# Optimization experiments

Hardware: AMD Instinct MI355X
Metric: run time of the kernel (lower is better)

The kernel has to match this reference:

```python
import jax, jax.numpy as jnp
import numpy as np

D_MODEL = 1024
NUM_HEADS = 16
D_K = D_MODEL // NUM_HEADS


def setup_inputs() -> dict:
    key = jax.random.key(0)
    kq, kk, kv, k1, k2, k3, k4 = jax.random.split(key, 7)
    B, S = 2, 2048
    # Xavier-uniform init for square [d_model, d_model] weights
    limit = float(np.sqrt(6.0 / (D_MODEL + D_MODEL)))
    def xav(k):
        return jax.random.uniform(k, (D_MODEL, D_MODEL), jnp.float32, -limit, limit)
    return {
        "query": jax.random.normal(kq, (B, S, D_MODEL), jnp.float32),
        "key": jax.random.normal(kk, (B, S, D_MODEL), jnp.float32),
        "value": jax.random.normal(kv, (B, S, D_MODEL), jnp.float32),
        "W_q": xav(k1),
        "W_k": xav(k2),
        "W_v": xav(k3),
        "W_o": xav(k4),
    }


def reference(query, key, value, W_q, W_k, W_v, W_o):
    B, Sq, _ = query.shape
    Sk = key.shape[1]
    # Linear layers: y = x @ W.T (torch nn.Linear convention)
    Q = (query @ W_q.T).reshape(B, Sq, NUM_HEADS, D_K).transpose(0, 2, 1, 3)
    K = (key @ W_k.T).reshape(B, Sk, NUM_HEADS, D_K).transpose(0, 2, 1, 3)
    V = (value @ W_v.T).reshape(B, Sk, NUM_HEADS, D_K).transpose(0, 2, 1, 3)
    scale = 1.0 / jnp.sqrt(jnp.asarray(D_K, Q.dtype))
    scores = jnp.einsum("bhqd,bhkd->bhqk", Q, K) * scale  # [B,H,Sq,Sk]
    attn = jax.nn.softmax(scores, axis=-1)
    # dropout is identity in eval mode
    out = jnp.einsum("bhqk,bhkd->bhqd", attn, V)
    out = out.transpose(0, 2, 1, 3).reshape(B, Sq, D_MODEL)
    return out @ W_o.T
```

## Files before the change

kernel.cpp:

```cpp
#include <hip/hip_runtime.h>
#include <math.h>

typedef unsigned short ushort_t;
typedef __attribute__((ext_vector_type(8))) short short8;
typedef __attribute__((ext_vector_type(4))) float f32x4;
typedef __attribute__((ext_vector_type(16))) float f32x16;
typedef __attribute__((ext_vector_type(4))) unsigned short ushort4v;
typedef __attribute__((ext_vector_type(2))) unsigned int uint2v;
typedef __attribute__((ext_vector_type(4))) unsigned int uint4v;

#define D_MODEL 1024
#define SEQ 2048
#define MROWS 4096
#define PLANE (MROWS * D_MODEL)
#define WELEM (D_MODEL * D_MODEL)

static __device__ __forceinline__ ushort_t f2bf(float f) {
    unsigned u = __builtin_bit_cast(unsigned, f);
    return (ushort_t)((u + 0x7fffu + ((u >> 16) & 1u)) >> 16);
}
static __device__ __forceinline__ unsigned cvtpk(float lo, float hi) {
    unsigned r;
    asm("v_cvt_pk_bf16_f32 %0, %1, %2" : "=v"(r) : "v"(lo), "v"(hi));
    return r;
}
static __device__ __forceinline__ short8 cvt8(float4 a, float4 b) {
    uint4v u = {cvtpk(a.x, a.y), cvtpk(a.z, a.w),
                cvtpk(b.x, b.y), cvtpk(b.z, b.w)};
    return __builtin_bit_cast(short8, u);
}

#define GLDS16(gp, lp)                                                         \
    __builtin_amdgcn_global_load_lds(                                          \
        (const __attribute__((address_space(1))) void*)(gp),                   \
        (__attribute__((address_space(3))) void*)(lp), 16, 0, 0)

__global__ __launch_bounds__(256)
void cvt_w(const float* __restrict__ w0, const float* __restrict__ w1,
           const float* __restrict__ w2, const float* __restrict__ w3,
           ushort_t* __restrict__ dst) {
    const int p = blockIdx.x >> 9;
    const float* s = (p == 0) ? w0 : (p == 1) ? w1 : (p == 2) ? w2 : w3;
    const int i = (((int)blockIdx.x & 511) * 256 + threadIdx.x) * 8;
    float4 a = *(const float4*)(s + i);
    float4 bb = *(const float4*)(s + i + 4);
    *(short8*)(dst + (size_t)p * WELEM + i) = cvt8(a, bb);
}

__global__ __launch_bounds__(256, 6)
void gemm3(const float* __restrict__ Xq, const float* __restrict__ Xk,
           const float* __restrict__ Xv, const ushort_t* __restrict__ Wb,
           ushort_t* __restrict__ Cb) {
    __shared__ __align__(16) ushort_t As[64 * 64];
    __shared__ __align__(16) ushort_t Bs[128 * 64];

    const int lin = blockIdx.x + blockIdx.y * 8 + blockIdx.z * 512;
    const int lin2 = (lin & 7) * 192 + (lin >> 3);
    const int z = lin2 >> 9;
    const int rem = lin2 & 511;
    const int by = rem >> 3;
    const int bx = rem & 7;

    const float* A = (z == 0) ? Xq : (z == 1) ? Xk : Xv;
    const ushort_t* B = Wb + (size_t)z * WELEM;
    ushort_t* C = Cb + (size_t)z * PLANE;

    const int tid = threadIdx.x;
    const int lane = tid & 63;
    const int wid = tid >> 6;
    const int wr = wid >> 1, wc = wid & 1;
    const int brow = by * 64;
    const int bcol = bx * 128;

    const int lrow = lane >> 3;
    const int g8 = lane & 7;
    const int loff = (g8 ^ lrow) * 8;

    const float* aF[2];
#pragma unroll
    for (int i = 0; i < 2; ++i)
        aF[i] = A + (size_t)(brow + wid * 16 + i * 8 + lrow) * D_MODEL + loff;
    const ushort_t* bS[4];
#pragma unroll
    for (int i = 0; i < 4; ++i)
        bS[i] = B + (size_t)(bcol + wid * 32 + i * 8 + lrow) * D_MODEL + loff;

    f32x4 acc[2][4];
#pragma unroll
    for (int i = 0; i < 2; ++i)
#pragma unroll
        for (int j = 0; j < 4; ++j) acc[i][j] = {0.f, 0.f, 0.f, 0.f};

    const int fr = lane & 15, fg = lane >> 4;

    float4 ar[2][2];
#pragma unroll
    for (int i = 0; i < 2; ++i) {
        ar[i][0] = *(const float4*)(aF[i]);
        ar[i][1] = *(const float4*)(aF[i] + 4);
    }

    for (int k0 = 0; k0 < D_MODEL; k0 += 64) {
        __syncthreads();
#pragma unroll
        for (int i = 0; i < 2; ++i)
            *(short8*)&As[(wid * 16 + i * 8 + lrow) * 64 + g8 * 8] =
                cvt8(ar[i][0], ar[i][1]);
#pragma unroll
        for (int i = 0; i < 4; ++i)
            GLDS16(bS[i] + k0, Bs + (wid * 32 + i * 8) * 64);
        if (k0 + 64 < D_MODEL) {
#pragma unroll
            for (int i = 0; i < 2; ++i) {
                ar[i][0] = *(const float4*)(aF[i] + k0 + 64);
                ar[i][1] = *(const float4*)(aF[i] + k0 + 68);
            }
        }
        __syncthreads();
#pragma unroll
        for (int ks = 0; ks < 2; ++ks) {
            const int coff = (ks * 32 + fg * 8) ^ ((fr & 7) << 3);
            short8 af[2], bw[4];
#pragma unroll
            for (int mi = 0; mi < 2; ++mi)
                af[mi] = *(const short8*)&As[(wr * 32 + mi * 16 + fr) * 64 + coff];
#pragma unroll
            for (int nj = 0; nj < 4; ++nj)
                bw[nj] = *(const short8*)&Bs[(wc * 64 + nj * 16 + fr) * 64 + coff];
#pragma unroll
            for (int mi = 0; mi < 2; ++mi)
#pragma unroll
                for (int nj = 0; nj < 4; ++nj)
                    acc[mi][nj] = __builtin_amdgcn_mfma_f32_16x16x32_bf16(
                        af[mi], bw[nj], acc[mi][nj], 0, 0, 0);
        }
    }

    if (z < 2) {
#pragma unroll
        for (int mi = 0; mi < 2; ++mi)
#pragma unroll
            for (int nj = 0; nj < 4; ++nj) {
                const int n = bcol + wc * 64 + nj * 16 + fr;
#pragma unroll
                for (int r = 0; r < 4; ++r) {
                    const int m = brow + wr * 32 + mi * 16 + fg * 4 + r;
                    C[(size_t)m * D_MODEL + n] = f2bf(acc[mi][nj][r]);
                }
            }
    } else {
#pragma unroll
        for (int mi = 0; mi < 2; ++mi)
#pragma unroll
            for (int nj = 0; nj < 4; ++nj) {
                const int n = bcol + wc * 64 + nj * 16 + fr;
                const int m0 = brow + wr * 32 + mi * 16 + fg * 4;
                ushort4v o4;
#pragma unroll
                for (int r = 0; r < 4; ++r) o4[r] = f2bf(acc[mi][nj][r]);
                *(ushort4v*)&C[((size_t)(m0 >> 11) << 21) + (size_t)n * SEQ + (m0 & 2047)] = o4;
            }
    }
}

__global__ __launch_bounds__(256)
void gemm_out(const ushort_t* __restrict__ A, const ushort_t* __restrict__ B,
              float* __restrict__ C) {
    __shared__ __align__(16) ushort_t As[2][128 * 64];
    __shared__ __align__(16) ushort_t Bs[2][64 * 64];

    const int lin = blockIdx.x + blockIdx.y * 16;
    const int lin2 = (lin & 7) * 64 + (lin >> 3);
    const int by = lin2 >> 4;
    const int bx = lin2 & 15;

    const int tid = threadIdx.x;
    const int lane = tid & 63;
    const int wid = tid >> 6;
    const int wr = wid >> 1, wc = wid & 1;
    const int brow = by * 128;
    const int bcol = bx * 64;

    const int lrow = lane >> 3;
    const int loff = ((lane & 7) ^ lrow) * 8;

    const ushort_t* aSrc[4];
    const ushort_t* bSrc[2];
#pragma unroll
    for (int i = 0; i < 4; ++i)
        aSrc[i] = A + (size_t)(brow + (wid * 4 + i) * 8 + lrow) * D_MODEL + loff;
#pragma unroll
    for (int i = 0; i < 2; ++i)
        bSrc[i] = B + (size_t)(bcol + (wid * 2 + i) * 8 + lrow) * D_MODEL + loff;

    f32x4 acc[4][2];
#pragma unroll
    for (int i = 0; i < 4; ++i)
#pragma unroll
        for (int j = 0; j < 2; ++j) acc[i][j] = {0.f, 0.f, 0.f, 0.f};

    const int fr = lane & 15, fg = lane >> 4;

#pragma unroll
    for (int i = 0; i < 4; ++i) GLDS16(aSrc[i], As[0] + (wid * 4 + i) * 512);
#pragma unroll
    for (int i = 0; i < 2; ++i) GLDS16(bSrc[i], Bs[0] + (wid * 2 + i) * 512);

    int cur = 0;
    for (int k0 = 0; k0 < D_MODEL; k0 += 64) {
        __syncthreads();
        if (k0 + 64 < D_MODEL) {
#pragma unroll
            for (int i = 0; i < 4; ++i)
                GLDS16(aSrc[i] + k0 + 64, As[cur ^ 1] + (wid * 4 + i) * 512);
#pragma unroll
            for (int i = 0; i < 2; ++i)
                GLDS16(bSrc[i] + k0 + 64, Bs[cur ^ 1] + (wid * 2 + i) * 512);
        }
#pragma unroll
        for (int ks = 0; ks < 2; ++ks) {
            const int coff = (ks * 32 + fg * 8) ^ ((fr & 7) << 3);
            short8 af[4], bw[2];
#pragma unroll
            for (int mi = 0; mi < 4; ++mi)
                af[mi] = *(const short8*)&As[cur][(wr * 64 + mi * 16 + fr) * 64 + coff];
#pragma unroll
            for (int nj = 0; nj < 2; ++nj)
                bw[nj] = *(const short8*)&Bs[cur][(wc * 32 + nj * 16 + fr) * 64 + coff];
#pragma unroll
            for (int mi = 0; mi < 4; ++mi)
#pragma unroll
                for (int nj = 0; nj < 2; ++nj)
                    acc[mi][nj] = __builtin_amdgcn_mfma_f32_16x16x32_bf16(
                        af[mi], bw[nj], acc[mi][nj], 0, 0, 0);
        }
        cur ^= 1;
    }

#pragma unroll
    for (int mi = 0; mi < 4; ++mi)
#pragma unroll
        for (int nj = 0; nj < 2; ++nj) {
            const int n = bcol + wc * 32 + nj * 16 + fr;
#pragma unroll
            for (int r = 0; r < 4; ++r) {
                const int m = brow + wr * 64 + mi * 16 + fg * 4 + r;
                C[(size_t)m * D_MODEL + n] = acc[mi][nj][r];
            }
        }
}

__global__ __launch_bounds__(512, 4)
void attn_mfma(const ushort_t* __restrict__ Qp, const ushort_t* __restrict__ Kp,
               const ushort_t* __restrict__ VT, ushort_t* __restrict__ Ap) {
    __shared__ __align__(16) ushort_t KB[4][4096];
    __shared__ __align__(16) ushort_t VB[4][4096];
    __shared__ float sm[2][128];
    __shared__ float sl[2][128];

    const int tid = threadIdx.x;
    const int lane = tid & 63;
    const int wid = tid >> 6;
    const int qgrp = wid & 3;
    const int khalf = wid >> 2;

    const int bid0 = blockIdx.x;
    const int bid = (bid0 & 7) * 64 + (bid0 >> 3);
    const int qt = bid & 15;
    const int h = (bid >> 4) & 15;
    const int b = bid >> 8;

    const int lrow = lane >> 3;
    const int loff = ((lane & 7) ^ lrow) * 8;
    const int q31 = lane & 31;
    const int hi = lane >> 5;

    const int m0 = b * SEQ + qt * 128;

    ushort_t* Qstage = &KB[2][0];
#pragma unroll
    for (int j = 0; j < 2; ++j) {
        const ushort_t* qS =
            Qp + (size_t)(m0 + wid * 16 + j * 8 + lrow) * D_MODEL + h * 64 + loff;
        GLDS16(qS, Qstage + (wid * 16 + j * 8) * 64);
    }
    const ushort_t* kS =
        Kp + (size_t)(b * SEQ + wid * 8 + lrow) * D_MODEL + h * 64 + loff;
    const ushort_t* vS =
        VT + ((size_t)b << 21) + (size_t)(h * 64 + wid * 8 + lrow) * SEQ + loff;
    GLDS16(kS, KB[0] + wid * 512);
    GLDS16(vS, VB[0] + wid * 512);
    kS += 64 * D_MODEL;
    vS += 64;
    GLDS16(kS, KB[1] + wid * 512);
    GLDS16(vS, VB[1] + wid * 512);
    kS += 64 * D_MODEL;
    vS += 64;
    __syncthreads();

    const int qrow = qgrp * 32 + q31;
    const int rsw = q31 & 7;
    short8 aq[4];
#pragma unroll
    for (int s = 0; s < 4; ++s)
        aq[s] = *(const short8*)&Qstage[qrow * 64 + (((s * 2 + hi) ^ rsw) * 8)];
    __syncthreads();

    f32x16 accO[2];
#pragma unroll
    for (int db = 0; db < 2; ++db)
#pragma unroll
        for (int r = 0; r < 16; ++r) accO[db][r] = 0.f;
    float m_s = -INFINITY;
    float l_p = 0.f;

    const float CEXP = 0.18033688011112042f;
    const int kbase = khalf * 32;

    int cur = 0;
    for (int st = 0; st < SEQ / 128; ++st) {
        if (st + 1 < SEQ / 128) {
            const int b0 = (cur ^ 1) * 2;
            GLDS16(kS, KB[b0] + wid * 512);
            GLDS16(vS, VB[b0] + wid * 512);
            kS += 64 * D_MODEL;
            vS += 64;
            GLDS16(kS, KB[b0 + 1] + wid * 512);
            GLDS16(vS, VB[b0 + 1] + wid * 512);
            kS += 64 * D_MODEL;
            vS += 64;
        }

#pragma unroll
        for (int sub = 0; sub < 2; ++sub) {
            const int bufi = cur * 2 + sub;

            f32x16 accS;
#pragma unroll
            for (int r = 0; r < 16; ++r) accS[r] = 0.f;
            __builtin_amdgcn_s_setprio(1);
#pragma unroll
            for (int s = 0; s < 4; ++s) {
                short8 ak = *(const short8*)&KB[bufi][(kbase + q31) * 64 +
                                                     (((s * 2 + hi) ^ rsw) * 8)];
                accS = __builtin_amdgcn_mfma_f32_32x32x16_bf16(ak, aq[s], accS, 0, 0, 0);
            }
            __builtin_amdgcn_s_setprio(0);

            float mx = accS[0];
#pragma unroll
            for (int r = 1; r < 16; ++r) mx = fmaxf(mx, accS[r]);
            mx = fmaxf(mx, __shfl_xor(mx, 32));
            const float cand = mx * CEXP;
            if (__any(cand > m_s + 8.f)) {
                const float mnew = fmaxf(m_s, cand);
                const float al = __builtin_amdgcn_exp2f(m_s - mnew);
                m_s = mnew;
                l_p *= al;
#pragma unroll
                for (int db = 0; db < 2; ++db)
#pragma unroll
                    for (int r = 0; r < 16; ++r) accO[db][r] *= al;
            }
            float ps = 0.f;
            const float nm = -m_s;
#pragma unroll
            for (int r = 0; r < 16; ++r) {
                const float p = __builtin_amdgcn_exp2f(fmaf(accS[r], CEXP, nm));
                accS[r] = p;
                ps += p;
            }
            l_p += ps;

            short8 pf[2];
#pragma unroll
            for (int ks2 = 0; ks2 < 2; ++ks2) {
                const int bse = ks2 * 8;
                unsigned w0 = cvtpk(accS[bse + 0], accS[bse + 1]);
                unsigned w1 = cvtpk(accS[bse + 2], accS[bse + 3]);
                unsigned w2 = cvtpk(accS[bse + 4], accS[bse + 5]);
                unsigned w3 = cvtpk(accS[bse + 6], accS[bse + 7]);
                asm("v_permlane32_swap_b32 %0, %1" : "+v"(w0), "+v"(w2));
                asm("v_permlane32_swap_b32 %0, %1" : "+v"(w1), "+v"(w3));
                uint4v u = {w0, w1, w2, w3};
                pf[ks2] = __builtin_bit_cast(short8, u);
            }

            __builtin_amdgcn_s_setprio(1);
#pragma unroll
            for (int db = 0; db < 2; ++db)
#pragma unroll
                for (int ks2 = 0; ks2 < 2; ++ks2) {
                    short8 av = *(const short8*)&VB[bufi][(db * 32 + q31) * 64 +
                        (((khalf * 4 + ks2 * 2 + hi) ^ rsw) * 8)];
                    accO[db] = __builtin_amdgcn_mfma_f32_32x32x16_bf16(
                        av, pf[ks2], accO[db], 0, 0, 0);
                }
            __builtin_amdgcn_s_setprio(0);
        }
        cur ^= 1;
        __syncthreads();
    }

    const float lt = l_p + __shfl_xor(l_p, 32);
    const int qg = qgrp * 32 + q31;
    if (lane < 32) {
        sm[khalf][qg] = m_s;
        sl[khalf][qg] = lt;
    }
    __syncthreads();
    const float mA = sm[0][qg], mB = sm[1][qg];
    const float mC = fmaxf(mA, mB);
    const float wA = __builtin_amdgcn_exp2f(mA - mC);
    const float wB = __builtin_amdgcn_exp2f(mB - mC);
    const float inv = 1.0f / (wA * sl[0][qg] + wB * sl[1][qg]);

    float* O1 = (float*)KB;
    if (khalf == 1) {
#pragma unroll
        for (int db = 0; db < 2; ++db)
#pragma unroll
            for (int rq = 0; rq < 4; ++rq) {
                f32x4 v;
#pragma unroll
                for (int j = 0; j < 4; ++j) v[j] = accO[db][rq * 4 + j] * wB;
                const int c = db * 8 + rq * 2 + hi;
                *(f32x4*)&O1[qg * 64 + ((c ^ (q31 & 15)) * 4)] = v;
            }
    }
    __syncthreads();
    unsigned* QsW = (unsigned*)VB;
    if (khalf == 0) {
        const int kkw = 2 * (q31 & 15);
#pragma unroll
        for (int db = 0; db < 2; ++db)
#pragma unroll
            for (int rq = 0; rq < 4; ++rq) {
                const int c = db * 8 + rq * 2 + hi;
                f32x4 o1 = *(const f32x4*)&O1[qg * 64 + ((c ^ (q31 & 15)) * 4)];
                float o0 = (accO[db][rq * 4 + 0] * wA + o1[0]) * inv;
                float o1v = (accO[db][rq * 4 + 1] * wA + o1[1]) * inv;
                float o2 = (accO[db][rq * 4 + 2] * wA + o1[2]) * inv;
                float o3 = (accO[db][rq * 4 + 3] * wA + o1[3]) * inv;
                uint2v u = {cvtpk(o0, o1v), cvtpk(o2, o3)};
                const int c0 = 4 * rq + 2 * hi + 16 * db;
                *(uint2v*)&QsW[qg * 32 + (c0 ^ kkw)] = u;
            }
    }
    __syncthreads();
#pragma unroll
    for (int pass = 0; pass < 2; ++pass) {
        const int r = wid * 16 + pass * 8 + (lane >> 3);
        const int g8 = lane & 7;
        const int kk = 2 * (r & 15);
        uint2v u0 = *(const uint2v*)&QsW[r * 32 + ((4 * g8) ^ kk)];
        uint2v u1 = *(const uint2v*)&QsW[r * 32 + ((4 * g8 + 2) ^ kk)];
        uint4v o = {u0[0], u0[1], u1[0], u1[1]};
        *(uint4v*)&Ap[(size_t)(m0 + r) * D_MODEL + h * 64 + g8 * 8] = o;
    }
}

extern "C" void kernel_launch(void* const* d_in, const int* in_sizes, int n_in,
                              void* d_out, int out_size, void* d_ws, size_t ws_size,
                              hipStream_t stream) {
    const float* query = (const float*)d_in[0];
    const float* key   = (const float*)d_in[1];
    const float* value = (const float*)d_in[2];
    const float* W_q   = (const float*)d_in[3];
    const float* W_k   = (const float*)d_in[4];
    const float* W_v   = (const float*)d_in[5];
    const float* W_o   = (const float*)d_in[6];
    float* out = (float*)d_out;

    ushort_t* ws = (ushort_t*)d_ws;
    ushort_t* Wb = ws + 3 * (size_t)PLANE;
    ushort_t* Qp = ws + 4 * (size_t)PLANE;
    ushort_t* Kp = Qp + (size_t)PLANE;
    ushort_t* VT = Kp + (size_t)PLANE;
    ushort_t* Ap = VT + (size_t)PLANE;

    cvt_w<<<2048, 256, 0, stream>>>(W_q, W_k, W_v, W_o, Wb);

    dim3 g3(D_MODEL / 128, MROWS / 64, 3);
    gemm3<<<g3, 256, 0, stream>>>(query, key, value, Wb, Qp);

    attn_mfma<<<512, 512, 0, stream>>>(Qp, Kp, VT, Ap);

    dim3 go(D_MODEL / 64, MROWS / 128);
    gemm_out<<<go, 256, 0, stream>>>(Ap, Wb + 3 * (size_t)WELEM, out);
}
```

Measured before the change: 116.7 us.

## Shrink projection GEMM tiles to 64x64 and drop double buffering in output GEMM

Both the QKV projection GEMM and the output GEMM now use 64x64 block tiles, which doubles the block count to fill more CUs and allows higher occupancy (launch bounds of 8 blocks). The output GEMM drops its double-buffered LDS prefetch for a single buffer with two barriers per k-step and relies on occupancy to hide latency. In exchange, smaller tiles lower arithmetic intensity and add global and LDS traffic per FLOP, and the lost overlap in the output GEMM may expose load latency.

```diff
diff --git a/kernel.cpp b/kernel.cpp
--- a/kernel.cpp
+++ b/kernel.cpp
@@ -47,19 +47,19 @@
     *(short8*)(dst + (size_t)p * WELEM + i) = cvt8(a, bb);
 }
 
-__global__ __launch_bounds__(256, 6)
+__global__ __launch_bounds__(256, 8)
 void gemm3(const float* __restrict__ Xq, const float* __restrict__ Xk,
            const float* __restrict__ Xv, const ushort_t* __restrict__ Wb,
            ushort_t* __restrict__ Cb) {
     __shared__ __align__(16) ushort_t As[64 * 64];
-    __shared__ __align__(16) ushort_t Bs[128 * 64];
-
-    const int lin = blockIdx.x + blockIdx.y * 8 + blockIdx.z * 512;
-    const int lin2 = (lin & 7) * 192 + (lin >> 3);
-    const int z = lin2 >> 9;
-    const int rem = lin2 & 511;
-    const int by = rem >> 3;
-    const int bx = rem & 7;
+    __shared__ __align__(16) ushort_t Bs[64 * 64];
+
+    const int lin = blockIdx.x + blockIdx.y * 16 + blockIdx.z * 1024;
+    const int lin2 = (lin & 7) * 384 + (lin >> 3);
+    const int z = lin2 >> 10;
+    const int rem = lin2 & 1023;
+    const int by = rem >> 4;
+    const int bx = rem & 15;
 
     const float* A = (z == 0) ? Xq : (z == 1) ? Xk : Xv;
     const ushort_t* B = Wb + (size_t)z * WELEM;
@@ -70,26 +70,25 @@
     const int wid = tid >> 6;
     const int wr = wid >> 1, wc = wid & 1;
     const int brow = by * 64;
-    const int bcol = bx * 128;
+    const int bcol = bx * 64;
 
     const int lrow = lane >> 3;
     const int g8 = lane & 7;
     const int loff = (g8 ^ lrow) * 8;
 
     const float* aF[2];
+    const ushort_t* bS[2];
+#pragma unroll
+    for (int i = 0; i < 2; ++i) {
+        aF[i] = A + (size_t)(brow + wid * 16 + i * 8 + lrow) * D_MODEL + loff;
+        bS[i] = B + (size_t)(bcol + wid * 16 + i * 8 + lrow) * D_MODEL + loff;
+    }
+
+    f32x4 acc[2][2];
 #pragma unroll
     for (int i = 0; i < 2; ++i)
-        aF[i] = A + (size_t)(brow + wid * 16 + i * 8 + lrow) * D_MODEL + loff;
-    const ushort_t* bS[4];
-#pragma unroll
-    for (int i = 0; i < 4; ++i)
-        bS[i] = B + (size_t)(bcol + wid * 32 + i * 8 + lrow) * D_MODEL + loff;
-
-    f32x4 acc[2][4];
-#pragma unroll
-    for (int i = 0; i < 2; ++i)
-#pragma unroll
-        for (int j = 0; j < 4; ++j) acc[i][j] = {0.f, 0.f, 0.f, 0.f};
+#pragma unroll
+        for (int j = 0; j < 2; ++j) acc[i][j] = {0.f, 0.f, 0.f, 0.f};
 
     const int fr = lane & 15, fg = lane >> 4;
 
@@ -103,12 +102,11 @@
     for (int k0 = 0; k0 < D_MODEL; k0 += 64) {
         __syncthreads();
 #pragma unroll
-        for (int i = 0; i < 2; ++i)
+        for (int i = 0; i < 2; ++i) {
             *(short8*)&As[(wid * 16 + i * 8 + lrow) * 64 + g8 * 8] =
                 cvt8(ar[i][0], ar[i][1]);
-#pragma unroll
-        for (int i = 0; i < 4; ++i)
-            GLDS16(bS[i] + k0, Bs + (wid * 32 + i * 8) * 64);
+            GLDS16(bS[i] + k0, Bs + (wid * 16 + i * 8) * 64);
+        }
         if (k0 + 64 < D_MODEL) {
 #pragma unroll
             for (int i = 0; i < 2; ++i) {
@@ -120,17 +118,17 @@
 #pragma unroll
         for (int ks = 0; ks < 2; ++ks) {
             const int coff = (ks * 32 + fg * 8) ^ ((fr & 7) << 3);
-            short8 af[2], bw[4];
+            short8 af[2], bw[2];
 #pragma unroll
             for (int mi = 0; mi < 2; ++mi)
                 af[mi] = *(const short8*)&As[(wr * 32 + mi * 16 + fr) * 64 + coff];
 #pragma unroll
-            for (int nj = 0; nj < 4; ++nj)
-                bw[nj] = *(const short8*)&Bs[(wc * 64 + nj * 16 + fr) * 64 + coff];
+            for (int nj = 0; nj < 2; ++nj)
+                bw[nj] = *(const short8*)&Bs[(wc * 32 + nj * 16 + fr) * 64 + coff];
 #pragma unroll
             for (int mi = 0; mi < 2; ++mi)
 #pragma unroll
-                for (int nj = 0; nj < 4; ++nj)
+                for (int nj = 0; nj < 2; ++nj)
                     acc[mi][nj] = __builtin_amdgcn_mfma_f32_16x16x32_bf16(
                         af[mi], bw[nj], acc[mi][nj], 0, 0, 0);
         }
@@ -140,8 +138,8 @@
 #pragma unroll
         for (int mi = 0; mi < 2; ++mi)
 #pragma unroll
-            for (int nj = 0; nj < 4; ++nj) {
-                const int n = bcol + wc * 64 + nj * 16 + fr;
+            for (int nj = 0; nj < 2; ++nj) {
+                const int n = bcol + wc * 32 + nj * 16 + fr;
 #pragma unroll
                 for (int r = 0; r < 4; ++r) {
                     const int m = brow + wr * 32 + mi * 16 + fg * 4 + r;
@@ -152,8 +150,8 @@
 #pragma unroll
         for (int mi = 0; mi < 2; ++mi)
 #pragma unroll
-            for (int nj = 0; nj < 4; ++nj) {
-                const int n = bcol + wc * 64 + nj * 16 + fr;
+            for (int nj = 0; nj < 2; ++nj) {
+                const int n = bcol + wc * 32 + nj * 16 + fr;
                 const int m0 = brow + wr * 32 + mi * 16 + fg * 4;
                 ushort4v o4;
 #pragma unroll
@@ -163,14 +161,14 @@
     }
 }
 
-__global__ __launch_bounds__(256)
+__global__ __launch_bounds__(256, 8)
 void gemm_out(const ushort_t* __restrict__ A, const ushort_t* __restrict__ B,
               float* __restrict__ C) {
-    __shared__ __align__(16) ushort_t As[2][128 * 64];
-    __shared__ __align__(16) ushort_t Bs[2][64 * 64];
+    __shared__ __align__(16) ushort_t As[64 * 64];
+    __shared__ __align__(16) ushort_t Bs[64 * 64];
 
     const int lin = blockIdx.x + blockIdx.y * 16;
-    const int lin2 = (lin & 7) * 64 + (lin >> 3);
+    const int lin2 = (lin & 7) * 128 + (lin >> 3);
     const int by = lin2 >> 4;
     const int bx = lin2 & 15;
 
@@ -178,73 +176,63 @@
     const int lane = tid & 63;
     const int wid = tid >> 6;
     const int wr = wid >> 1, wc = wid & 1;
-    const int brow = by * 128;
+    const int brow = by * 64;
     const int bcol = bx * 64;
 
     const int lrow = lane >> 3;
     const int loff = ((lane & 7) ^ lrow) * 8;
 
-    const ushort_t* aSrc[4];
-    const ushort_t* bSrc[2];
-#pragma unroll
-    for (int i = 0; i < 4; ++i)
-        aSrc[i] = A + (size_t)(brow + (wid * 4 + i) * 8 + lrow) * D_MODEL + loff;
+    const ushort_t* aS[2];
+    const ushort_t* bS[2];
+#pragma unroll
+    for (int i = 0; i < 2; ++i) {
+        aS[i] = A + (size_t)(brow + wid * 16 + i * 8 + lrow) * D_MODEL + loff;
+        bS[i] = B + (size_t)(bcol + wid * 16 + i * 8 + lrow) * D_MODEL + loff;
+    }
+
+    f32x4 acc[2][2];
 #pragma unroll
     for (int i = 0; i < 2; ++i)
-        bSrc[i] = B + (size_t)(bcol + (wid * 2 + i) * 8 + lrow) * D_MODEL + loff;
-
-    f32x4 acc[4][2];
-#pragma unroll
-    for (int i = 0; i < 4; ++i)
 #pragma unroll
         for (int j = 0; j < 2; ++j) acc[i][j] = {0.f, 0.f, 0.f, 0.f};
 
     const int fr = lane & 15, fg = lane >> 4;
 
-#pragma unroll
-    for (int i = 0; i < 4; ++i) GLDS16(aSrc[i], As[0] + (wid * 4 + i) * 512);
-#pragma unroll
-    for (int i = 0; i < 2; ++i) GLDS16(bSrc[i], Bs[0] + (wid * 2 + i) * 512);
-
-    int cur = 0;
     for (int k0 = 0; k0 < D_MODEL; k0 += 64) {
         __syncthreads();
-        if (k0 + 64 < D_MODEL) {
-#pragma unroll
-            for (int i = 0; i < 4; ++i)
-                GLDS16(aSrc[i] + k0 + 64, As[cur ^ 1] + (wid * 4 + i) * 512);
-#pragma unroll
-            for (int i = 0; i < 2; ++i)
-                GLDS16(bSrc[i] + k0 + 64, Bs[cur ^ 1] + (wid * 2 + i) * 512);
-        }
+#pragma unroll
+        for (int i = 0; i < 2; ++i) {
+            GLDS16(aS[i] + k0, As + (wid * 16 + i * 8) * 64);
+            GLDS16(bS[i] + k0, Bs + (wid * 16 + i * 8) * 64);
+        }
+        __syncthreads();
 #pragma unroll
         for (int ks = 0; ks < 2; ++ks) {
             const int coff = (ks * 32 + fg * 8) ^ ((fr & 7) << 3);
-            short8 af[4], bw[2];
-#pragma unroll
-            for (int mi = 0; mi < 4; ++mi)
-                af[mi] = *(const short8*)&As[cur][(wr * 64 + mi * 16 + fr) * 64 + coff];
+            short8 af[2], bw[2];
+#pragma unroll
+            for (int mi = 0; mi < 2; ++mi)
+                af[mi] = *(const short8*)&As[(wr * 32 + mi * 16 + fr) * 64 + coff];
 #pragma unroll
             for (int nj = 0; nj < 2; ++nj)
-                bw[nj] = *(const short8*)&Bs[cur][(wc * 32 + nj * 16 + fr) * 64 + coff];
-#pragma unroll
-            for (int mi = 0; mi < 4; ++mi)
+                bw[nj] = *(const short8*)&Bs[(wc * 32 + nj * 16 + fr) * 64 + coff];
+#pragma unroll
+            for (int mi = 0; mi < 2; ++mi)
 #pragma unroll
                 for (int nj = 0; nj < 2; ++nj)
                     acc[mi][nj] = __builtin_amdgcn_mfma_f32_16x16x32_bf16(
                         af[mi], bw[nj], acc[mi][nj], 0, 0, 0);
         }
-        cur ^= 1;
-    }
-
-#pragma unroll
-    for (int mi = 0; mi < 4; ++mi)
+    }
+
+#pragma unroll
+    for (int mi = 0; mi < 2; ++mi)
 #pragma unroll
         for (int nj = 0; nj < 2; ++nj) {
             const int n = bcol + wc * 32 + nj * 16 + fr;
 #pragma unroll
             for (int r = 0; r < 4; ++r) {
-                const int m = brow + wr * 64 + mi * 16 + fg * 4 + r;
+                const int m = brow + wr * 32 + mi * 16 + fg * 4 + r;
                 C[(size_t)m * D_MODEL + n] = acc[mi][nj][r];
             }
         }
@@ -481,11 +469,11 @@
 
     cvt_w<<<2048, 256, 0, stream>>>(W_q, W_k, W_v, W_o, Wb);
 
-    dim3 g3(D_MODEL / 128, MROWS / 64, 3);
+    dim3 g3(D_MODEL / 64, MROWS / 64, 3);
     gemm3<<<g3, 256, 0, stream>>>(query, key, value, Wb, Qp);
 
     attn_mfma<<<512, 512, 0, stream>>>(Qp, Kp, VT, Ap);
 
-    dim3 go(D_MODEL / 64, MROWS / 128);
+    dim3 go(D_MODEL / 64, MROWS / 64);
     gemm_out<<<go, 256, 0, stream>>>(Ap, Wb + 3 * (size_t)WELEM, out);
 }
```

Measured after the change: 123.7 us. +6.0%, slower.
